# Optimization experiments

Measured on AMD Instinct MI355X. Metric: run time of the kernel, lower is better.

## Reference

```python
import jax, jax.numpy as jnp
import numpy as np

B, LQ, LK, D = 8, 2048, 2048, 128

def setup_inputs() -> dict:
    key = jax.random.key(0)
    k1, k2, k3, k4 = jax.random.split(key, 4)
    return {
        "query": jax.random.normal(k1, (B, LQ, D), dtype=jnp.float32),
        "key": jax.random.normal(k2, (B, LK, D), dtype=jnp.float32),
        "value": jax.random.normal(k3, (B, LK, D), dtype=jnp.float32),
        "scale_factor": jax.random.normal(k4, (B, LQ, LK), dtype=jnp.float32),
    }

def reference(query, key, value, scale_factor):
    # qk: [B, LQ, LK]
    qk = jnp.einsum("bqd,bkd->bqk", query, key)
    probs = jax.nn.softmax(qk * scale_factor, axis=-1)
    # dropout_p = 0.0 -> identity
    return jnp.einsum("bqk,bkd->bqd", probs, value)
```

## Files before the change

kernel.cpp:

```cpp
#include <hip/hip_runtime.h>
#include <hip/hip_bf16.h>


typedef float          f32x4 __attribute__((ext_vector_type(4)));
typedef short          s16x8 __attribute__((ext_vector_type(8)));
typedef unsigned int   u32x4 __attribute__((ext_vector_type(4)));
typedef unsigned short u16x4 __attribute__((ext_vector_type(4)));

#define LOG2E 1.4426950408889634f

__device__ __forceinline__ float fast_exp2(float x) {
#if __has_builtin(__builtin_amdgcn_exp2f)
    return __builtin_amdgcn_exp2f(x);
#else
    return exp2f(x);
#endif
}

__device__ __forceinline__ unsigned short f2bf(float x) {
    return __builtin_bit_cast(unsigned short, __float2bfloat16(x));
}
__device__ __forceinline__ float bf2f(unsigned short u) {
    return __bfloat162float(__builtin_bit_cast(__hip_bfloat16, u));
}

__global__ void prep(const float* __restrict__ q,
                     const float* __restrict__ k,
                     const float* __restrict__ v,
                     unsigned short* __restrict__ qh,
                     unsigned short* __restrict__ ql,
                     unsigned short* __restrict__ kh,
                     unsigned short* __restrict__ kl,
                     unsigned short* __restrict__ vt) {
    __shared__ unsigned short tile[64 * 132];
    const int bb  = blockIdx.x;
    const int tid = threadIdx.x;

    if (bb < 4096) {
        const bool isq = bb < 2048;
        const float* src = isq ? q : k;
        unsigned short* hi = isq ? qh : kh;
        unsigned short* lo = isq ? ql : kl;
        const int i = (isq ? bb : bb - 2048) * 256 + tid;
        const float4 val = ((const float4*)src)[i];
        float f[4] = {val.x, val.y, val.z, val.w};
        u16x4 h, l;
#pragma unroll
        for (int j = 0; j < 4; ++j) {
            unsigned short hb = f2bf(f[j]);
            h[j] = hb;
            l[j] = f2bf(f[j] - bf2f(hb));
        }
        ((u16x4*)hi)[i] = h;
        ((u16x4*)lo)[i] = l;
        return;
    }

    const int tb = bb - 4096;
    const int b  = tb & 7;
    const int k0 = (tb >> 3) * 64;
#pragma unroll
    for (int p = 0; p < 8; ++p) {
        int idx  = p * 256 + tid;
        int kk   = idx >> 5;
        int dblk = idx & 31;
        float4 val = ((const float4*)v)[((b * 2048 + k0 + kk) * 128 + dblk * 4) >> 2];
        u16x4 t4;
        t4[0] = f2bf(val.x); t4[1] = f2bf(val.y);
        t4[2] = f2bf(val.z); t4[3] = f2bf(val.w);
        *(u16x4*)&tile[kk * 132 + dblk * 4] = t4;
    }
    __syncthreads();
#pragma unroll
    for (int p = 0; p < 4; ++p) {
        int idx = p * 256 + tid;
        int d   = idx >> 3;
        int k8  = idx & 7;
        u16x4 a, c;
#pragma unroll
        for (int j = 0; j < 4; ++j) a[j] = tile[(k8 * 8 + j) * 132 + d];
#pragma unroll
        for (int j = 0; j < 4; ++j) c[j] = tile[(k8 * 8 + 4 + j) * 132 + d];
        unsigned short* outp = vt + (b * 128 + d) * 2048 + k0 + k8 * 8;
        *(u16x4*)outp       = a;
        *(u16x4*)(outp + 4) = c;
    }
}

#define KHS 136
#define VTS 40
#define PS  40

template <int KSPLIT>
__global__ __launch_bounds__(256, 4)
void flash_fwd(const unsigned short* __restrict__ qh_g,
               const unsigned short* __restrict__ ql_g,
               const unsigned short* __restrict__ kh_g,
               const unsigned short* __restrict__ kl_g,
               const unsigned short* __restrict__ vt_g,
               const float* __restrict__ scale_g,
               float* __restrict__ opart,
               float* __restrict__ mpart,
               float* __restrict__ lpart) {
    __shared__ unsigned short lds_kh[32 * KHS];
    __shared__ unsigned short lds_kl[32 * KHS];
    __shared__ unsigned short lds_vt[128 * VTS];
    __shared__ unsigned short lds_p[4][16 * PS];

    const int tid  = threadIdx.x;
    const int wave = tid >> 6;
    const int lane = tid & 63;
    const int c    = lane & 15;
    const int g    = lane >> 4;

    const int bid   = blockIdx.x;
    const int b     = bid & 7;
    const int qt    = (bid >> 3) & 31;
    const int ks    = bid >> 8;
    const int q0    = qt * 64;
    const int kbase = ks * (2048 / KSPLIT);
    const int NIT   = 2048 / KSPLIT / 32;

    const int srow = tid >> 4, sc8 = tid & 15;
    const int sdv  = tid >> 2, sk4 = tid & 3;

    s16x8 qh[4], ql[4];
    {
        const int qrow = b * 2048 + q0 + wave * 16 + c;
#pragma unroll
        for (int kstep = 0; kstep < 4; ++kstep) {
            int idx = qrow * 16 + kstep * 4 + g;
            qh[kstep] = __builtin_bit_cast(s16x8, ((const u32x4*)qh_g)[idx]);
            ql[kstep] = __builtin_bit_cast(s16x8, ((const u32x4*)ql_g)[idx]);
        }
    }

    f32x4 oacc[8];
#pragma unroll
    for (int t = 0; t < 8; ++t) oacc[t] = (f32x4){0.f, 0.f, 0.f, 0.f};
    float m2[4], ln[4];
#pragma unroll
    for (int r = 0; r < 4; ++r) { m2[r] = -INFINITY; ln[r] = 0.f; }

    u32x4 pk[2], pl[2], pv[2];
    float scn[2][4];
    const int scb = (b * 2048 + q0 + wave * 16 + g * 4) * 2048 + c;

    {
        const int k0 = kbase;
#pragma unroll
        for (int p = 0; p < 2; ++p) {
            int gidx = (b * 2048 + k0 + p * 16 + srow) * 16 + sc8;
            pk[p] = ((const u32x4*)kh_g)[gidx];
            pl[p] = ((const u32x4*)kl_g)[gidx];
            int vidx = (b * 128 + p * 64 + sdv) * 256 + (k0 >> 3) + sk4;
            pv[p] = ((const u32x4*)vt_g)[vidx];
        }
#pragma unroll
        for (int t = 0; t < 2; ++t)
#pragma unroll
            for (int r = 0; r < 4; ++r)
                scn[t][r] = scale_g[scb + r * 2048 + k0 + t * 16];
    }

    for (int kc = 0; kc < NIT; ++kc) {
        const int k0 = kbase + kc * 32;

        __syncthreads();
#pragma unroll
        for (int p = 0; p < 2; ++p) {
            *(u32x4*)&lds_kh[(p * 16 + srow) * KHS + sc8 * 8] = pk[p];
            *(u32x4*)&lds_kl[(p * 16 + srow) * KHS + sc8 * 8] = pl[p];
            *(u32x4*)&lds_vt[(p * 64 + sdv) * VTS + sk4 * 8]  = pv[p];
        }
        __syncthreads();

        float sc[2][4];
#pragma unroll
        for (int t = 0; t < 2; ++t)
#pragma unroll
            for (int r = 0; r < 4; ++r)
                sc[t][r] = scn[t][r] * LOG2E;

        if (kc < NIT - 1) {
            const int kn = k0 + 32;
#pragma unroll
            for (int p = 0; p < 2; ++p) {
                int gidx = (b * 2048 + kn + p * 16 + srow) * 16 + sc8;
                pk[p] = ((const u32x4*)kh_g)[gidx];
                pl[p] = ((const u32x4*)kl_g)[gidx];
                int vidx = (b * 128 + p * 64 + sdv) * 256 + (kn >> 3) + sk4;
                pv[p] = ((const u32x4*)vt_g)[vidx];
            }
#pragma unroll
            for (int t = 0; t < 2; ++t)
#pragma unroll
                for (int r = 0; r < 4; ++r)
                    scn[t][r] = scale_g[scb + r * 2048 + kn + t * 16];
        }

        f32x4 s[2];
#pragma unroll
        for (int t = 0; t < 2; ++t) s[t] = (f32x4){0.f, 0.f, 0.f, 0.f};
#pragma unroll
        for (int kstep = 0; kstep < 4; ++kstep) {
#pragma unroll
            for (int t = 0; t < 2; ++t) {
                int off = (t * 16 + c) * KHS + kstep * 32 + g * 8;
                s16x8 bh = *(const s16x8*)&lds_kh[off];
                s16x8 bl = *(const s16x8*)&lds_kl[off];
                s[t] = __builtin_amdgcn_mfma_f32_16x16x32_bf16(qh[kstep], bh, s[t], 0, 0, 0);
                s[t] = __builtin_amdgcn_mfma_f32_16x16x32_bf16(ql[kstep], bh, s[t], 0, 0, 0);
                s[t] = __builtin_amdgcn_mfma_f32_16x16x32_bf16(qh[kstep], bl, s[t], 0, 0, 0);
            }
        }

        float lt[2][4], mx[4];
#pragma unroll
        for (int r = 0; r < 4; ++r) {
            lt[0][r] = s[0][r] * sc[0][r];
            lt[1][r] = s[1][r] * sc[1][r];
            mx[r] = fmaxf(lt[0][r], lt[1][r]);
        }
#pragma unroll
        for (int mask = 1; mask < 16; mask <<= 1)
#pragma unroll
            for (int r = 0; r < 4; ++r)
                mx[r] = fmaxf(mx[r], __shfl_xor(mx[r], mask));
        float al[4], rs[4];
#pragma unroll
        for (int r = 0; r < 4; ++r) {
            float mn = fmaxf(m2[r], mx[r]);
            al[r] = fast_exp2(m2[r] - mn);
            m2[r] = mn;
            rs[r] = 0.f;
        }
#pragma unroll
        for (int t = 0; t < 2; ++t)
#pragma unroll
            for (int r = 0; r < 4; ++r) {
                float p = fast_exp2(lt[t][r] - m2[r]);
                rs[r] += p;
                lds_p[wave][(g * 4 + r) * PS + t * 16 + c] = f2bf(p);
            }
#pragma unroll
        for (int mask = 1; mask < 16; mask <<= 1)
#pragma unroll
            for (int r = 0; r < 4; ++r)
                rs[r] += __shfl_xor(rs[r], mask);
#pragma unroll
        for (int r = 0; r < 4; ++r) ln[r] = ln[r] * al[r] + rs[r];
#pragma unroll
        for (int t = 0; t < 8; ++t)
#pragma unroll
            for (int r = 0; r < 4; ++r) oacc[t][r] *= al[r];

        {
            s16x8 af = *(const s16x8*)&lds_p[wave][c * PS + g * 8];
#pragma unroll
            for (int t2 = 0; t2 < 8; ++t2) {
                s16x8 bv = *(const s16x8*)&lds_vt[(t2 * 16 + c) * VTS + g * 8];
                oacc[t2] = __builtin_amdgcn_mfma_f32_16x16x32_bf16(af, bv, oacc[t2], 0, 0, 0);
            }
        }
    }

    {
        const int rowb = (ks * 8 + b) * 2048 + q0 + wave * 16;
#pragma unroll
        for (int t2 = 0; t2 < 8; ++t2)
#pragma unroll
            for (int r = 0; r < 4; ++r)
                opart[(size_t)(rowb + g * 4 + r) * 128 + t2 * 16 + c] = oacc[t2][r];
        if (c == 0) {
#pragma unroll
            for (int r = 0; r < 4; ++r) {
                mpart[rowb + g * 4 + r] = m2[r];
                lpart[rowb + g * 4 + r] = ln[r];
            }
        }
    }
}

template <int KSPLIT>
__global__ void merge_parts(const float* __restrict__ opart,
                            const float* __restrict__ mpart,
                            const float* __restrict__ lpart,
                            float* __restrict__ out) {
    const int row = blockIdx.x;
    const int d   = threadIdx.x;
    float m[KSPLIT], l[KSPLIT];
    float M = -INFINITY;
#pragma unroll
    for (int i = 0; i < KSPLIT; ++i) {
        m[i] = mpart[i * 16384 + row];
        l[i] = lpart[i * 16384 + row];
        M = fmaxf(M, m[i]);
    }
    float denom = 0.f, acc = 0.f;
    const size_t base = (size_t)row * 128 + d;
#pragma unroll
    for (int i = 0; i < KSPLIT; ++i) {
        const float a = fast_exp2(m[i] - M);
        denom += a * l[i];
        acc   += a * opart[(size_t)i * 16384 * 128 + base];
    }
    out[base] = acc / denom;
}

extern "C" void kernel_launch(void* const* d_in, const int* in_sizes, int n_in,
                              void* d_out, int out_size, void* d_ws, size_t ws_size,
                              hipStream_t stream) {
    const float* q  = (const float*)d_in[0];
    const float* k  = (const float*)d_in[1];
    const float* v  = (const float*)d_in[2];
    const float* sc = (const float*)d_in[3];
    float* out = (float*)d_out;

    char* ws = (char*)d_ws;
    const size_t MB = 1024 * 1024;
    unsigned short* qh = (unsigned short*)(ws);
    unsigned short* ql = (unsigned short*)(ws + 4 * MB);
    unsigned short* kh = (unsigned short*)(ws + 8 * MB);
    unsigned short* kl = (unsigned short*)(ws + 12 * MB);
    unsigned short* vt = (unsigned short*)(ws + 16 * MB);

    prep<<<4352, 256, 0, stream>>>(q, k, v, qh, ql, kh, kl, vt);

    const size_t need4 = 20 * MB + (size_t)4 * 16384 * 128 * 4 + (size_t)2 * 4 * 16384 * 4;
    if (ws_size >= need4) {
        float* opart = (float*)(ws + 20 * MB);
        float* mpart = (float*)(ws + 52 * MB);
        float* lpart = (float*)(ws + 52 * MB + 256 * 1024);
        flash_fwd<4><<<1024, 256, 0, stream>>>(qh, ql, kh, kl, vt, sc, opart, mpart, lpart);
        merge_parts<4><<<16384, 128, 0, stream>>>(opart, mpart, lpart, out);
    } else {
        float* opart = (float*)(ws + 20 * MB);
        float* mpart = (float*)(ws + 36 * MB);
        float* lpart = (float*)(ws + 36 * MB + 128 * 1024);
        flash_fwd<2><<<512, 256, 0, stream>>>(qh, ql, kh, kl, vt, sc, opart, mpart, lpart);
        merge_parts<2><<<16384, 128, 0, stream>>>(opart, mpart, lpart, out);
    }
}
```

Measured before the change: 271.2 us.

## Transpose QK MFMA to keep P in registers, widen key tile, split by three

Computes S with K as the A operand so each lane holds a query column, which lets the softmax probabilities feed the PV MFMA straight from registers. This removes the per-wave LDS staging of P and cuts the row reductions to two cross-group shuffles. The key tile doubles to 64 with vectorized float4 scale loads, and the key dimension is split into three uneven chunks with occupancy lowered to three blocks per CU. The risks are higher register and LDS pressure and fewer blocks in flight.

```diff
diff --git a/kernel.cpp b/kernel.cpp
--- a/kernel.cpp
+++ b/kernel.cpp
@@ -88,11 +88,10 @@
 }
 
 #define KHS 136
-#define VTS 40
-#define PS  40
+#define VTS 72
 
 template <int KSPLIT>
-__global__ __launch_bounds__(256, 4)
+__global__ __launch_bounds__(256, 3)
 void flash_fwd(const unsigned short* __restrict__ qh_g,
                const unsigned short* __restrict__ ql_g,
                const unsigned short* __restrict__ kh_g,
@@ -102,10 +101,9 @@
                float* __restrict__ opart,
                float* __restrict__ mpart,
                float* __restrict__ lpart) {
-    __shared__ unsigned short lds_kh[32 * KHS];
-    __shared__ unsigned short lds_kl[32 * KHS];
+    __shared__ unsigned short lds_kh[64 * KHS];
+    __shared__ unsigned short lds_kl[64 * KHS];
     __shared__ unsigned short lds_vt[128 * VTS];
-    __shared__ unsigned short lds_p[4][16 * PS];
 
     const int tid  = threadIdx.x;
     const int wave = tid >> 6;
@@ -118,11 +116,16 @@
     const int qt    = (bid >> 3) & 31;
     const int ks    = bid >> 8;
     const int q0    = qt * 64;
-    const int kbase = ks * (2048 / KSPLIT);
-    const int NIT   = 2048 / KSPLIT / 32;
+
+    const int PER   = (32 + KSPLIT - 1) / KSPLIT;
+    const int kt0   = ks * PER;
+    const int NIT   = min(PER, 32 - kt0);
+    const int kbase = kt0 * 64;
 
     const int srow = tid >> 4, sc8 = tid & 15;
-    const int sdv  = tid >> 2, sk4 = tid & 3;
+    const int sdv  = tid >> 3, sk8 = tid & 7;
+
+    const int rc = 8 * (c >> 2) + (c & 3);
 
     s16x8 qh[4], ql[4];
     {
@@ -138,129 +141,158 @@
     f32x4 oacc[8];
 #pragma unroll
     for (int t = 0; t < 8; ++t) oacc[t] = (f32x4){0.f, 0.f, 0.f, 0.f};
-    float m2[4], ln[4];
-#pragma unroll
-    for (int r = 0; r < 4; ++r) { m2[r] = -INFINITY; ln[r] = 0.f; }
-
-    u32x4 pk[2], pl[2], pv[2];
-    float scn[2][4];
-    const int scb = (b * 2048 + q0 + wave * 16 + g * 4) * 2048 + c;
+    float m2 = -INFINITY, ln = 0.f;
+
+    u32x4 pk[4], pl[4], pv[4];
+    float4 scn[4];
+    const size_t scb = (size_t)(b * 2048 + q0 + wave * 16 + c) * 2048 + 8 * g;
 
     {
         const int k0 = kbase;
 #pragma unroll
-        for (int p = 0; p < 2; ++p) {
+        for (int p = 0; p < 4; ++p) {
             int gidx = (b * 2048 + k0 + p * 16 + srow) * 16 + sc8;
             pk[p] = ((const u32x4*)kh_g)[gidx];
             pl[p] = ((const u32x4*)kl_g)[gidx];
-            int vidx = (b * 128 + p * 64 + sdv) * 256 + (k0 >> 3) + sk4;
+            int vidx = (b * 128 + p * 32 + sdv) * 256 + (k0 >> 3) + sk8;
             pv[p] = ((const u32x4*)vt_g)[vidx];
         }
-#pragma unroll
-        for (int t = 0; t < 2; ++t)
-#pragma unroll
-            for (int r = 0; r < 4; ++r)
-                scn[t][r] = scale_g[scb + r * 2048 + k0 + t * 16];
+        scn[0] = *(const float4*)&scale_g[scb + k0 + 0];
+        scn[1] = *(const float4*)&scale_g[scb + k0 + 32];
+        scn[2] = *(const float4*)&scale_g[scb + k0 + 4];
+        scn[3] = *(const float4*)&scale_g[scb + k0 + 36];
     }
 
     for (int kc = 0; kc < NIT; ++kc) {
-        const int k0 = kbase + kc * 32;
+        const int k0 = kbase + kc * 64;
 
         __syncthreads();
 #pragma unroll
-        for (int p = 0; p < 2; ++p) {
+        for (int p = 0; p < 4; ++p) {
             *(u32x4*)&lds_kh[(p * 16 + srow) * KHS + sc8 * 8] = pk[p];
             *(u32x4*)&lds_kl[(p * 16 + srow) * KHS + sc8 * 8] = pl[p];
-            *(u32x4*)&lds_vt[(p * 64 + sdv) * VTS + sk4 * 8]  = pv[p];
+            *(u32x4*)&lds_vt[(p * 32 + sdv) * VTS + sk8 * 8]  = pv[p];
         }
         __syncthreads();
 
-        float sc[2][4];
-#pragma unroll
-        for (int t = 0; t < 2; ++t)
-#pragma unroll
-            for (int r = 0; r < 4; ++r)
-                sc[t][r] = scn[t][r] * LOG2E;
+        float scl[4][4];
+#pragma unroll
+        for (int t = 0; t < 4; ++t) {
+            scl[t][0] = scn[t].x * LOG2E; scl[t][1] = scn[t].y * LOG2E;
+            scl[t][2] = scn[t].z * LOG2E; scl[t][3] = scn[t].w * LOG2E;
+        }
 
         if (kc < NIT - 1) {
-            const int kn = k0 + 32;
-#pragma unroll
-            for (int p = 0; p < 2; ++p) {
+            const int kn = k0 + 64;
+#pragma unroll
+            for (int p = 0; p < 4; ++p) {
                 int gidx = (b * 2048 + kn + p * 16 + srow) * 16 + sc8;
                 pk[p] = ((const u32x4*)kh_g)[gidx];
                 pl[p] = ((const u32x4*)kl_g)[gidx];
-                int vidx = (b * 128 + p * 64 + sdv) * 256 + (kn >> 3) + sk4;
+                int vidx = (b * 128 + p * 32 + sdv) * 256 + (kn >> 3) + sk8;
                 pv[p] = ((const u32x4*)vt_g)[vidx];
             }
-#pragma unroll
-            for (int t = 0; t < 2; ++t)
-#pragma unroll
-                for (int r = 0; r < 4; ++r)
-                    scn[t][r] = scale_g[scb + r * 2048 + kn + t * 16];
-        }
-
-        f32x4 s[2];
-#pragma unroll
-        for (int t = 0; t < 2; ++t) s[t] = (f32x4){0.f, 0.f, 0.f, 0.f};
+            scn[0] = *(const float4*)&scale_g[scb + kn + 0];
+            scn[1] = *(const float4*)&scale_g[scb + kn + 32];
+            scn[2] = *(const float4*)&scale_g[scb + kn + 4];
+            scn[3] = *(const float4*)&scale_g[scb + kn + 36];
+        }
+
+        f32x4 s[4];
+#pragma unroll
+        for (int t = 0; t < 4; ++t) s[t] = (f32x4){0.f, 0.f, 0.f, 0.f};
 #pragma unroll
         for (int kstep = 0; kstep < 4; ++kstep) {
-#pragma unroll
-            for (int t = 0; t < 2; ++t) {
-                int off = (t * 16 + c) * KHS + kstep * 32 + g * 8;
-                s16x8 bh = *(const s16x8*)&lds_kh[off];
-                s16x8 bl = *(const s16x8*)&lds_kl[off];
-                s[t] = __builtin_amdgcn_mfma_f32_16x16x32_bf16(qh[kstep], bh, s[t], 0, 0, 0);
-                s[t] = __builtin_amdgcn_mfma_f32_16x16x32_bf16(ql[kstep], bh, s[t], 0, 0, 0);
-                s[t] = __builtin_amdgcn_mfma_f32_16x16x32_bf16(qh[kstep], bl, s[t], 0, 0, 0);
-            }
-        }
-
-        float lt[2][4], mx[4];
-#pragma unroll
-        for (int r = 0; r < 4; ++r) {
-            lt[0][r] = s[0][r] * sc[0][r];
-            lt[1][r] = s[1][r] * sc[1][r];
-            mx[r] = fmaxf(lt[0][r], lt[1][r]);
-        }
-#pragma unroll
-        for (int mask = 1; mask < 16; mask <<= 1)
-#pragma unroll
-            for (int r = 0; r < 4; ++r)
-                mx[r] = fmaxf(mx[r], __shfl_xor(mx[r], mask));
-        float al[4], rs[4];
-#pragma unroll
-        for (int r = 0; r < 4; ++r) {
-            float mn = fmaxf(m2[r], mx[r]);
-            al[r] = fast_exp2(m2[r] - mn);
-            m2[r] = mn;
-            rs[r] = 0.f;
-        }
-#pragma unroll
-        for (int t = 0; t < 2; ++t)
+            const int co = kstep * 32 + g * 8;
+            {
+                s16x8 bh = *(const s16x8*)&lds_kh[(rc + 0) * KHS + co];
+                s16x8 bl = *(const s16x8*)&lds_kl[(rc + 0) * KHS + co];
+                s[0] = __builtin_amdgcn_mfma_f32_16x16x32_bf16(bh, qh[kstep], s[0], 0, 0, 0);
+                s[0] = __builtin_amdgcn_mfma_f32_16x16x32_bf16(bh, ql[kstep], s[0], 0, 0, 0);
+                s[0] = __builtin_amdgcn_mfma_f32_16x16x32_bf16(bl, qh[kstep], s[0], 0, 0, 0);
+            }
+            {
+                s16x8 bh = *(const s16x8*)&lds_kh[(rc + 32) * KHS + co];
+                s16x8 bl = *(const s16x8*)&lds_kl[(rc + 32) * KHS + co];
+                s[1] = __builtin_amdgcn_mfma_f32_16x16x32_bf16(bh, qh[kstep], s[1], 0, 0, 0);
+                s[1] = __builtin_amdgcn_mfma_f32_16x16x32_bf16(bh, ql[kstep], s[1], 0, 0, 0);
+                s[1] = __builtin_amdgcn_mfma_f32_16x16x32_bf16(bl, qh[kstep], s[1], 0, 0, 0);
+            }
+            {
+                s16x8 bh = *(const s16x8*)&lds_kh[(rc + 4) * KHS + co];
+                s16x8 bl = *(const s16x8*)&lds_kl[(rc + 4) * KHS + co];
+                s[2] = __builtin_amdgcn_mfma_f32_16x16x32_bf16(bh, qh[kstep], s[2], 0, 0, 0);
+                s[2] = __builtin_amdgcn_mfma_f32_16x16x32_bf16(bh, ql[kstep], s[2], 0, 0, 0);
+                s[2] = __builtin_amdgcn_mfma_f32_16x16x32_bf16(bl, qh[kstep], s[2], 0, 0, 0);
+            }
+            {
+                s16x8 bh = *(const s16x8*)&lds_kh[(rc + 36) * KHS + co];
+                s16x8 bl = *(const s16x8*)&lds_kl[(rc + 36) * KHS + co];
+                s[3] = __builtin_amdgcn_mfma_f32_16x16x32_bf16(bh, qh[kstep], s[3], 0, 0, 0);
+                s[3] = __builtin_amdgcn_mfma_f32_16x16x32_bf16(bh, ql[kstep], s[3], 0, 0, 0);
+                s[3] = __builtin_amdgcn_mfma_f32_16x16x32_bf16(bl, qh[kstep], s[3], 0, 0, 0);
+            }
+        }
+
+        float p[4][4];
+        float mx = -INFINITY;
+#pragma unroll
+        for (int t = 0; t < 4; ++t)
 #pragma unroll
             for (int r = 0; r < 4; ++r) {
-                float p = fast_exp2(lt[t][r] - m2[r]);
-                rs[r] += p;
-                lds_p[wave][(g * 4 + r) * PS + t * 16 + c] = f2bf(p);
-            }
-#pragma unroll
-        for (int mask = 1; mask < 16; mask <<= 1)
-#pragma unroll
-            for (int r = 0; r < 4; ++r)
-                rs[r] += __shfl_xor(rs[r], mask);
-#pragma unroll
-        for (int r = 0; r < 4; ++r) ln[r] = ln[r] * al[r] + rs[r];
-#pragma unroll
-        for (int t = 0; t < 8; ++t)
-#pragma unroll
-            for (int r = 0; r < 4; ++r) oacc[t][r] *= al[r];
+                float v = s[t][r] * scl[t][r];
+                p[t][r] = v;
+                mx = fmaxf(mx, v);
+            }
+        mx = fmaxf(mx, __shfl_xor(mx, 16));
+        mx = fmaxf(mx, __shfl_xor(mx, 32));
+        const float mn = fmaxf(m2, mx);
+        const float al = fast_exp2(m2 - mn);
+        m2 = mn;
+        float rs = 0.f;
+#pragma unroll
+        for (int t = 0; t < 4; ++t)
+#pragma unroll
+            for (int r = 0; r < 4; ++r) {
+                float pe = fast_exp2(p[t][r] - mn);
+                p[t][r] = pe;
+                rs += pe;
+            }
+        rs += __shfl_xor(rs, 16);
+        rs += __shfl_xor(rs, 32);
+        ln = ln * al + rs;
+
+        float alr[4];
+#pragma unroll
+        for (int r = 0; r < 4; ++r)
+            alr[r] = __shfl(al, (lane & 48) | (g * 4 + r));
+#pragma unroll
+        for (int t2 = 0; t2 < 8; ++t2)
+#pragma unroll
+            for (int r = 0; r < 4; ++r) oacc[t2][r] *= alr[r];
+
+        unsigned int w[8];
+#pragma unroll
+        for (int t = 0; t < 4; ++t)
+#pragma unroll
+            for (int h = 0; h < 2; ++h)
+                w[t * 2 + h] = (unsigned int)f2bf(p[t][2 * h]) |
+                               ((unsigned int)f2bf(p[t][2 * h + 1]) << 16);
+        u32x4 af0 = {w[0], w[1], w[4], w[5]};
+        u32x4 af1 = {w[2], w[3], w[6], w[7]};
 
         {
-            s16x8 af = *(const s16x8*)&lds_p[wave][c * PS + g * 8];
+            s16x8 a0 = __builtin_bit_cast(s16x8, af0);
 #pragma unroll
             for (int t2 = 0; t2 < 8; ++t2) {
                 s16x8 bv = *(const s16x8*)&lds_vt[(t2 * 16 + c) * VTS + g * 8];
-                oacc[t2] = __builtin_amdgcn_mfma_f32_16x16x32_bf16(af, bv, oacc[t2], 0, 0, 0);
+                oacc[t2] = __builtin_amdgcn_mfma_f32_16x16x32_bf16(a0, bv, oacc[t2], 0, 0, 0);
+            }
+            s16x8 a1 = __builtin_bit_cast(s16x8, af1);
+#pragma unroll
+            for (int t2 = 0; t2 < 8; ++t2) {
+                s16x8 bv = *(const s16x8*)&lds_vt[(t2 * 16 + c) * VTS + 32 + g * 8];
+                oacc[t2] = __builtin_amdgcn_mfma_f32_16x16x32_bf16(a1, bv, oacc[t2], 0, 0, 0);
             }
         }
     }
@@ -272,12 +304,9 @@
 #pragma unroll
             for (int r = 0; r < 4; ++r)
                 opart[(size_t)(rowb + g * 4 + r) * 128 + t2 * 16 + c] = oacc[t2][r];
-        if (c == 0) {
-#pragma unroll
-            for (int r = 0; r < 4; ++r) {
-                mpart[rowb + g * 4 + r] = m2[r];
-                lpart[rowb + g * 4 + r] = ln[r];
-            }
+        if (g == 0) {
+            mpart[rowb + c] = m2;
+            lpart[rowb + c] = ln;
         }
     }
 }
@@ -327,13 +356,13 @@
 
     prep<<<4352, 256, 0, stream>>>(q, k, v, qh, ql, kh, kl, vt);
 
-    const size_t need4 = 20 * MB + (size_t)4 * 16384 * 128 * 4 + (size_t)2 * 4 * 16384 * 4;
-    if (ws_size >= need4) {
+    const size_t need3 = 44 * MB + 512 * 1024;
+    if (ws_size >= need3) {
         float* opart = (float*)(ws + 20 * MB);
-        float* mpart = (float*)(ws + 52 * MB);
-        float* lpart = (float*)(ws + 52 * MB + 256 * 1024);
-        flash_fwd<4><<<1024, 256, 0, stream>>>(qh, ql, kh, kl, vt, sc, opart, mpart, lpart);
-        merge_parts<4><<<16384, 128, 0, stream>>>(opart, mpart, lpart, out);
+        float* mpart = (float*)(ws + 44 * MB);
+        float* lpart = (float*)(ws + 44 * MB + 256 * 1024);
+        flash_fwd<3><<<768, 256, 0, stream>>>(qh, ql, kh, kl, vt, sc, opart, mpart, lpart);
+        merge_parts<3><<<16384, 128, 0, stream>>>(opart, mpart, lpart, out);
     } else {
         float* opart = (float*)(ws + 20 * MB);
         float* mpart = (float*)(ws + 36 * MB);
```

Result: slower. 310.9 us (+14.6%).
